# Kernel tuning notes

Hardware: AMD Instinct MI355X
Metric: run time of the kernel (lower is better)

The kernel has to match this reference:

```python
import jax, jax.numpy as jnp
import numpy as np

N_ENT = 100000
N_REL = 500
N_EDGES = 800000
IN_DIM = 128
OUT_DIM = 128


def setup_inputs() -> dict:
    key = jax.random.key(0)
    ks = jax.random.split(key, 7)
    heads = jax.random.randint(ks[0], (N_EDGES,), 0, N_ENT)
    tails = jax.random.randint(ks[1], (N_EDGES,), 0, N_ENT)
    rels = jax.random.randint(ks[2], (N_EDGES,), 0, N_REL)
    triplets = jnp.stack([heads, tails, rels], axis=1)  # [E, 3] (head, tail, rel)
    ent_embed = jax.random.normal(ks[3], (N_ENT, IN_DIM), dtype=jnp.float32)
    rel_embed = jax.random.normal(ks[4], (N_REL, IN_DIM), dtype=jnp.float32)
    # xavier_normal with gain=1.414 for both linear weights; zero biases (torch default bias init is uniform, but scale is tiny)
    Wa = jax.random.normal(ks[5], (OUT_DIM, 3 * IN_DIM), dtype=jnp.float32) * (1.414 * np.sqrt(2.0 / (3 * IN_DIM + OUT_DIM)))
    Wa2 = jax.random.normal(ks[6], (1, OUT_DIM), dtype=jnp.float32) * (1.414 * np.sqrt(2.0 / (OUT_DIM + 1)))
    ba = jnp.zeros((OUT_DIM,), dtype=jnp.float32)
    ba2 = jnp.zeros((1,), dtype=jnp.float32)
    return {"triplets": triplets, "ent_embed": ent_embed, "rel_embed": rel_embed,
            "Wa": Wa, "ba": ba, "Wa2": Wa2, "ba2": ba2}


def reference(triplets, ent_embed, rel_embed, Wa, ba, Wa2, ba2):
    heads = triplets[:, 0]
    tails = triplets[:, 1]
    rels = triplets[:, 2]
    # gather per-edge features: [E, 3*in_dim]
    h = jnp.concatenate([ent_embed[heads], rel_embed[rels], ent_embed[tails]], axis=1)
    c = h @ Wa.T + ba                      # [E, out_dim]
    b = jax.nn.leaky_relu(c @ Wa2.T + ba2)  # [E, 1], slope 0.01 (torch default)
    e_b = jnp.exp(b)                       # [E, 1]
    # torch builds sparse COO (head, rel) tensors, detaches, and sums over dim=1:
    # that is exactly a segment-sum over head node. detach -> stop_gradient.
    ebs = jax.ops.segment_sum(jax.lax.stop_gradient(e_b), heads, num_segments=N_ENT)       # [N, 1]
    hs = jax.ops.segment_sum(jax.lax.stop_gradient(e_b * c), heads, num_segments=N_ENT)    # [N, out_dim]
    ebs = jnp.where(ebs == 0.0, jnp.float32(1e-12), ebs)
    out = hs / ebs
    return jax.nn.elu(out)  # concat=True branch
```

## Files before the change

### kernel.cpp

```cpp
#include <hip/hip_runtime.h>

#define N_ENT   100000
#define N_REL   500
#define N_EDGES 800000
#define DIM     128
#define WA_LD   384

#define MT       256
#define ENT_BLKS ((N_ENT + MT - 1) / MT)
#define REL_BLKS 63
#define CAP      64

#define SCW 264

typedef __attribute__((ext_vector_type(8))) short  s8v;
typedef __attribute__((ext_vector_type(4))) float  f4v;

__device__ __forceinline__ unsigned short f2bf(float x) {
    unsigned u = __float_as_uint(x);
    return (unsigned short)((u + 0x7FFFu + ((u >> 16) & 1u)) >> 16);
}
__device__ __forceinline__ float bf2f(unsigned short h) {
    return __uint_as_float(((unsigned)h) << 16);
}

__global__ __launch_bounds__(256) void k_prep(const float* __restrict__ Wa,
                                              short* __restrict__ Bg) {
    int idx = blockIdx.x * 256 + threadIdx.x;
    int tt = idx >> 11;
    int g = idx & 2047;
    int j = g >> 4;
    int k8 = g & 15;
    const float* src = Wa + (size_t)j * WA_LD + tt * 256 + k8 * 8;
    float4 v0 = *(const float4*)src;
    float4 v1 = *(const float4*)(src + 4);
    float x[8] = {v0.x, v0.y, v0.z, v0.w, v1.x, v1.y, v1.z, v1.w};
    s8v hv;
#pragma unroll
    for (int e = 0; e < 8; ++e) hv[e] = (short)f2bf(x[e]);
    int col = tt * 128 + j;
    int kc = k8 >> 2;
    int lanep = (k8 & 3) * 16 + (col & 15);
    int nt = col >> 4;
    *(s8v*)&Bg[((size_t)((kc * 16 + nt) * 64 + lanep)) * 8] = hv;
}

__global__ __launch_bounds__(512) void k_fused(const float* __restrict__ ent,
                                               const short* __restrict__ Bg,
                                               const float* __restrict__ Wa2,
                                               unsigned short* __restrict__ PHb,
                                               unsigned short* __restrict__ PTb,
                                               float* __restrict__ qh,
                                               float* __restrict__ qt,
                                               const float* __restrict__ rel,
                                               const float* __restrict__ Wa,
                                               const float* __restrict__ ba,
                                               float* __restrict__ PR,
                                               float* __restrict__ qr) {
    __shared__ __align__(16) unsigned short SCR[8 * 16 * SCW];
    __shared__ float relLds[8][128];
    s8v* BsV = (s8v*)SCR;
    int t = threadIdx.x;
    int wv = t >> 6;
    int lane = t & 63;

    if (blockIdx.x >= ENT_BLKS) {
        int rb = blockIdx.x - ENT_BLKS;
        int r = rb * 8 + wv;
        if (r < N_REL) {
            relLds[wv][lane]      = rel[r * DIM + lane];
            relLds[wv][64 + lane] = rel[r * DIM + 64 + lane];
            int j0 = 2 * lane, j1 = j0 + 1;
            const float* w0 = Wa + (size_t)j0 * WA_LD + 128;
            const float* w1 = Wa + (size_t)j1 * WA_LD + 128;
            float a0 = ba[j0], a1 = ba[j1];
#pragma unroll 8
            for (int k4 = 0; k4 < 32; ++k4) {
                float4 rv = *(const float4*)&relLds[wv][4 * k4];
                float4 x0 = *(const float4*)&w0[4 * k4];
                float4 x1 = *(const float4*)&w1[4 * k4];
                a0 += rv.x * x0.x + rv.y * x0.y + rv.z * x0.z + rv.w * x0.w;
                a1 += rv.x * x1.x + rv.y * x1.y + rv.z * x1.z + rv.w * x1.w;
            }
            *(float2*)&PR[(size_t)r * DIM + j0] = make_float2(a0, a1);
            float p = a0 * Wa2[j0] + a1 * Wa2[j1];
#pragma unroll
            for (int m = 1; m <= 32; m <<= 1) p += __shfl_xor(p, m);
            if (lane == 0) qr[r] = p;
        }
        return;
    }

#pragma unroll
    for (int it = 0; it < 8; ++it) {
        int idx = t + 512 * it;
        BsV[idx] = *(const s8v*)&Bg[(size_t)idx * 8];
    }

    int l15 = lane & 15, lg = lane >> 4;
    int m0 = blockIdx.x * MT + wv * 32;

    f4v acc[2][16];
#pragma unroll
    for (int s = 0; s < 2; ++s)
#pragma unroll
        for (int nt = 0; nt < 16; ++nt)
            acc[s][nt] = (f4v){0.f, 0.f, 0.f, 0.f};

    __syncthreads();

#pragma unroll
    for (int kc = 0; kc < 4; ++kc) {
        s8v Ah[2];
#pragma unroll
        for (int s = 0; s < 2; ++s) {
            int row = m0 + s * 16 + l15;
            if (row < N_ENT) {
                const float* ap = ent + (size_t)row * DIM + kc * 32 + lg * 8;
                float4 v0 = *(const float4*)ap;
                float4 v1 = *(const float4*)(ap + 4);
                float x[8] = {v0.x, v0.y, v0.z, v0.w, v1.x, v1.y, v1.z, v1.w};
#pragma unroll
                for (int e = 0; e < 8; ++e) Ah[s][e] = (short)f2bf(x[e]);
            } else {
                Ah[s] = (s8v){0, 0, 0, 0, 0, 0, 0, 0};
            }
        }
#pragma unroll
        for (int nt = 0; nt < 16; ++nt) {
            s8v bg = BsV[(kc * 16 + nt) * 64 + lane];
            acc[0][nt] = __builtin_amdgcn_mfma_f32_16x16x32_bf16(Ah[0], bg, acc[0][nt], 0, 0, 0);
            acc[1][nt] = __builtin_amdgcn_mfma_f32_16x16x32_bf16(Ah[1], bg, acc[1][nt], 0, 0, 0);
        }
    }

    float wa2v[8];
#pragma unroll
    for (int c8 = 0; c8 < 8; ++c8) wa2v[c8] = Wa2[c8 * 16 + l15];

#pragma unroll
    for (int s = 0; s < 2; ++s) {
        int rowb = m0 + s * 16 + lg * 4;
        float qhp[4] = {0.f, 0.f, 0.f, 0.f};
        float qtp[4] = {0.f, 0.f, 0.f, 0.f};
#pragma unroll
        for (int nt = 0; nt < 16; ++nt) {
#pragma unroll
            for (int g = 0; g < 4; ++g) {
                float v = acc[s][nt][g];
                if (nt < 8) qhp[g] += v * wa2v[nt];
                else        qtp[g] += v * wa2v[nt & 7];
            }
        }
#pragma unroll
        for (int g = 0; g < 4; ++g) {
            float a = qhp[g], b = qtp[g];
#pragma unroll
            for (int m = 1; m <= 8; m <<= 1) {
                a += __shfl_xor(a, m);
                b += __shfl_xor(b, m);
            }
            int row = rowb + g;
            if (l15 == 0 && row < N_ENT) { qh[row] = a; qt[row] = b; }
        }
    }

    __syncthreads();

    unsigned short* scr = &SCR[wv * 16 * SCW];
#pragma unroll
    for (int s = 0; s < 2; ++s) {
#pragma unroll
        for (int nt = 0; nt < 16; ++nt)
#pragma unroll
            for (int g = 0; g < 4; ++g)
                scr[(lg * 4 + g) * SCW + nt * 16 + l15] = f2bf(acc[s][nt][g]);
#pragma unroll
        for (int p = 0; p < 8; ++p) {
            int row16 = p * 2 + (lane >> 5);
            int col8  = lane & 31;
            s8v val = *(s8v*)&scr[row16 * SCW + col8 * 8];
            int row = m0 + s * 16 + row16;
            if (row < N_ENT) {
                unsigned short* dst = (col8 < 16 ? PHb : PTb)
                                    + (size_t)row * DIM + (col8 & 15) * 8;
                *(s8v*)dst = val;
            }
        }
    }
}

__global__ __launch_bounds__(256) void k_scatter(const int* __restrict__ trip,
                                                 const float* __restrict__ qh,
                                                 const float* __restrict__ qt,
                                                 const float* __restrict__ qr,
                                                 const float* __restrict__ ba2,
                                                 int* __restrict__ cnt,
                                                 float2* __restrict__ pkw) {
    __shared__ int tl3[768];
    __shared__ float qrs[N_REL];
    int t = threadIdx.x;
    for (int i = t; i < N_REL; i += 256) qrs[i] = qr[i];
    int e0blk = blockIdx.x * 256;
    int base3 = e0blk * 3;
#pragma unroll
    for (int i = t; i < 768; i += 256)
        tl3[i] = (base3 + i < N_EDGES * 3) ? trip[base3 + i] : 0;
    __syncthreads();
    int e = e0blk + t;
    if (e >= N_EDGES) return;
    int h  = tl3[t * 3 + 0];
    int tt = tl3[t * 3 + 1];
    int r  = tl3[t * 3 + 2];
    float b = qh[h] + qt[tt] + qrs[r] + ba2[0];
    float lr = b > 0.f ? b : 0.01f * b;
    float w = expf(lr);
    int pos = atomicAdd(&cnt[h], 1);
    if (pos < CAP) {
        float2 v;
        v.x = __uint_as_float(((unsigned)r << 17) | (unsigned)tt);
        v.y = w;
        pkw[(size_t)h * CAP + pos] = v;
    }
}

__global__ __launch_bounds__(256) void k_gather(const int* __restrict__ cnt,
                                                const float2* __restrict__ pkw,
                                                const unsigned short* __restrict__ PHb,
                                                const float* __restrict__ PR,
                                                const unsigned short* __restrict__ PTb,
                                                float* __restrict__ out) {
    int idx = blockIdx.x * 256 + threadIdx.x;
    int i = idx >> 5, lane = idx & 31;
    if (i >= N_ENT) return;
    int lane4 = lane * 4;
    int e0 = i * CAP;
    int n = cnt[i]; if (n > CAP) n = CAP;
    int e1 = e0 + n;
    float4 acc = make_float4(0.f, 0.f, 0.f, 0.f);
    float sw = 0.f;
    int e = e0;
    for (; e + 3 < e1; e += 4) {
        float2 pw0 = pkw[e],     pw1 = pkw[e + 1];
        float2 pw2 = pkw[e + 2], pw3 = pkw[e + 3];
        unsigned p0 = __float_as_uint(pw0.x), p1 = __float_as_uint(pw1.x);
        unsigned p2 = __float_as_uint(pw2.x), p3 = __float_as_uint(pw3.x);
        ushort4 b0 = *(const ushort4*)&PTb[(size_t)(p0 & 0x1FFFFu) * DIM + lane4];
        ushort4 b1 = *(const ushort4*)&PTb[(size_t)(p1 & 0x1FFFFu) * DIM + lane4];
        ushort4 b2 = *(const ushort4*)&PTb[(size_t)(p2 & 0x1FFFFu) * DIM + lane4];
        ushort4 b3 = *(const ushort4*)&PTb[(size_t)(p3 & 0x1FFFFu) * DIM + lane4];
        float4 r0 = *(const float4*)&PR[(size_t)(p0 >> 17) * DIM + lane4];
        float4 r1 = *(const float4*)&PR[(size_t)(p1 >> 17) * DIM + lane4];
        float4 r2 = *(const float4*)&PR[(size_t)(p2 >> 17) * DIM + lane4];
        float4 r3 = *(const float4*)&PR[(size_t)(p3 >> 17) * DIM + lane4];
        float w0 = pw0.y, w1 = pw1.y, w2 = pw2.y, w3 = pw3.y;
        acc.x += w0 * (r0.x + bf2f(b0.x)) + w1 * (r1.x + bf2f(b1.x))
               + w2 * (r2.x + bf2f(b2.x)) + w3 * (r3.x + bf2f(b3.x));
        acc.y += w0 * (r0.y + bf2f(b0.y)) + w1 * (r1.y + bf2f(b1.y))
               + w2 * (r2.y + bf2f(b2.y)) + w3 * (r3.y + bf2f(b3.y));
        acc.z += w0 * (r0.z + bf2f(b0.z)) + w1 * (r1.z + bf2f(b1.z))
               + w2 * (r2.z + bf2f(b2.z)) + w3 * (r3.z + bf2f(b3.z));
        acc.w += w0 * (r0.w + bf2f(b0.w)) + w1 * (r1.w + bf2f(b1.w))
               + w2 * (r2.w + bf2f(b2.w)) + w3 * (r3.w + bf2f(b3.w));
        sw += (w0 + w1) + (w2 + w3);
    }
    for (; e < e1; ++e) {
        float2 pw = pkw[e];
        unsigned p = __float_as_uint(pw.x);
        float w = pw.y;
        ushort4 b = *(const ushort4*)&PTb[(size_t)(p & 0x1FFFFu) * DIM + lane4];
        float4 pr = *(const float4*)&PR[(size_t)(p >> 17) * DIM + lane4];
        acc.x += w * (pr.x + bf2f(b.x));
        acc.y += w * (pr.y + bf2f(b.y));
        acc.z += w * (pr.z + bf2f(b.z));
        acc.w += w * (pr.w + bf2f(b.w));
        sw += w;
    }
    ushort4 hb = *(const ushort4*)&PHb[(size_t)i * DIM + lane4];
    acc.x += sw * bf2f(hb.x);
    acc.y += sw * bf2f(hb.y);
    acc.z += sw * bf2f(hb.z);
    acc.w += sw * bf2f(hb.w);
    float den = (sw == 0.f) ? 1e-12f : sw;
    float inv = 1.f / den;
    float vx = acc.x * inv, vy = acc.y * inv, vz = acc.z * inv, vw = acc.w * inv;
    vx = vx > 0.f ? vx : expm1f(vx);
    vy = vy > 0.f ? vy : expm1f(vy);
    vz = vz > 0.f ? vz : expm1f(vz);
    vw = vw > 0.f ? vw : expm1f(vw);
    *(float4*)&out[(size_t)i * DIM + lane4] = make_float4(vx, vy, vz, vw);
}

extern "C" void kernel_launch(void* const* d_in, const int* in_sizes, int n_in,
                              void* d_out, int out_size, void* d_ws, size_t ws_size,
                              hipStream_t stream) {
    const int*   trip = (const int*)d_in[0];
    const float* ent  = (const float*)d_in[1];
    const float* rel  = (const float*)d_in[2];
    const float* Wa   = (const float*)d_in[3];
    const float* ba   = (const float*)d_in[4];
    const float* Wa2  = (const float*)d_in[5];
    const float* ba2  = (const float*)d_in[6];
    float* out = (float*)d_out;

    float* ws = (float*)d_ws;
    size_t o = 0;
    unsigned short* PHb = (unsigned short*)(ws + o); o += (size_t)N_ENT * DIM / 2;
    unsigned short* PTb = (unsigned short*)(ws + o); o += (size_t)N_ENT * DIM / 2;
    float* PR = ws + o;        o += (size_t)N_REL * DIM;
    float* qh = ws + o;        o += N_ENT;
    float* qt = ws + o;        o += N_ENT;
    float* qr = ws + o;        o += N_REL + 4;
    short* Bg = (short*)(ws + o);     o += 32768 / 2 + 8;
    int*   cnt = (int*)(ws + o);      o += N_ENT;
    float2* pkw = (float2*)(ws + o);  o += (size_t)N_ENT * CAP * 2;

    hipMemsetAsync(cnt, 0, (size_t)N_ENT * sizeof(int), stream);

    k_prep<<<16, 256, 0, stream>>>(Wa, Bg);
    k_fused<<<ENT_BLKS + REL_BLKS, 512, 0, stream>>>(ent, Bg, Wa2, PHb, PTb, qh, qt,
                                                     rel, Wa, ba, PR, qr);
    k_scatter<<<(N_EDGES + 255) / 256, 256, 0, stream>>>(trip, qh, qt, qr, ba2, cnt, pkw);
    k_gather<<<(N_ENT * 32) / 256, 256, 0, stream>>>(cnt, pkw, PHb, PR, PTb, out);
}
```

Measured before the change: 137.5 us.

## Split fused entity GEMM into two N-halves with smaller blocks

The entity projection kernel now uses 256-thread blocks covering 128 rows. It preloads all A fragments into registers, then runs two passes that each stage half of the bf16 weight tiles in LDS and compute 8 output tiles. This halves the live accumulator count and shrinks LDS per block, aiming for higher occupancy and more blocks in flight. The cost is extra barriers, reloading B per pass, and holding the whole A row in registers.

```diff
diff --git a/kernel.cpp b/kernel.cpp
--- a/kernel.cpp
+++ b/kernel.cpp
@@ -6,12 +6,12 @@
 #define DIM     128
 #define WA_LD   384
 
-#define MT       256
+#define MT       128
 #define ENT_BLKS ((N_ENT + MT - 1) / MT)
-#define REL_BLKS 63
+#define REL_BLKS 125
 #define CAP      64
 
-#define SCW 264
+#define SCW 144
 
 typedef __attribute__((ext_vector_type(8))) short  s8v;
 typedef __attribute__((ext_vector_type(4))) float  f4v;
@@ -45,7 +45,7 @@
     *(s8v*)&Bg[((size_t)((kc * 16 + nt) * 64 + lanep)) * 8] = hv;
 }
 
-__global__ __launch_bounds__(512) void k_fused(const float* __restrict__ ent,
+__global__ __launch_bounds__(256) void k_fused(const float* __restrict__ ent,
                                                const short* __restrict__ Bg,
                                                const float* __restrict__ Wa2,
                                                unsigned short* __restrict__ PHb,
@@ -57,16 +57,16 @@
                                                const float* __restrict__ ba,
                                                float* __restrict__ PR,
                                                float* __restrict__ qr) {
-    __shared__ __align__(16) unsigned short SCR[8 * 16 * SCW];
-    __shared__ float relLds[8][128];
-    s8v* BsV = (s8v*)SCR;
+    __shared__ __align__(16) s8v Bs[2048];
+    __shared__ __align__(16) unsigned short SCR[4 * 16 * SCW];
+    __shared__ float relLds[4][128];
     int t = threadIdx.x;
     int wv = t >> 6;
     int lane = t & 63;
 
     if (blockIdx.x >= ENT_BLKS) {
         int rb = blockIdx.x - ENT_BLKS;
-        int r = rb * 8 + wv;
+        int r = rb * 4 + wv;
         if (r < N_REL) {
             relLds[wv][lane]      = rel[r * DIM + lane];
             relLds[wv][64 + lane] = rel[r * DIM + 64 + lane];
@@ -91,100 +91,101 @@
         return;
     }
 
-#pragma unroll
-    for (int it = 0; it < 8; ++it) {
-        int idx = t + 512 * it;
-        BsV[idx] = *(const s8v*)&Bg[(size_t)idx * 8];
-    }
-
     int l15 = lane & 15, lg = lane >> 4;
     int m0 = blockIdx.x * MT + wv * 32;
 
-    f4v acc[2][16];
-#pragma unroll
-    for (int s = 0; s < 2; ++s)
-#pragma unroll
-        for (int nt = 0; nt < 16; ++nt)
-            acc[s][nt] = (f4v){0.f, 0.f, 0.f, 0.f};
-
-    __syncthreads();
-
-#pragma unroll
-    for (int kc = 0; kc < 4; ++kc) {
-        s8v Ah[2];
+    s8v Af[2][4];
+#pragma unroll
+    for (int s = 0; s < 2; ++s) {
+        int row = m0 + s * 16 + l15;
+        if (row < N_ENT) {
+            const float* ap = ent + (size_t)row * DIM + lg * 8;
+#pragma unroll
+            for (int kc = 0; kc < 4; ++kc) {
+                float4 v0 = *(const float4*)(ap + kc * 32);
+                float4 v1 = *(const float4*)(ap + kc * 32 + 4);
+                float x[8] = {v0.x, v0.y, v0.z, v0.w, v1.x, v1.y, v1.z, v1.w};
+#pragma unroll
+                for (int e = 0; e < 8; ++e) Af[s][kc][e] = (short)f2bf(x[e]);
+            }
+        } else {
+#pragma unroll
+            for (int kc = 0; kc < 4; ++kc)
+                Af[s][kc] = (s8v){0, 0, 0, 0, 0, 0, 0, 0};
+        }
+    }
+
+    float wa2v[8];
+#pragma unroll
+    for (int c8 = 0; c8 < 8; ++c8) wa2v[c8] = Wa2[c8 * 16 + l15];
+
+    const s8v* Bg8 = (const s8v*)Bg;
+    unsigned short* scr = &SCR[wv * 16 * SCW];
+
+#pragma unroll
+    for (int pass = 0; pass < 2; ++pass) {
+#pragma unroll
+        for (int it = 0; it < 8; ++it) {
+            int g = t + 256 * it;
+            int tile = g >> 6, l = g & 63;
+            int kc = tile >> 3, ntl = tile & 7;
+            Bs[g] = Bg8[(kc * 16 + pass * 8 + ntl) * 64 + l];
+        }
+        __syncthreads();
+
+        f4v acc[2][8];
+#pragma unroll
+        for (int s = 0; s < 2; ++s)
+#pragma unroll
+            for (int nt = 0; nt < 8; ++nt)
+                acc[s][nt] = (f4v){0.f, 0.f, 0.f, 0.f};
+
+#pragma unroll
+        for (int kc = 0; kc < 4; ++kc)
+#pragma unroll
+            for (int nt = 0; nt < 8; ++nt) {
+                s8v bg = Bs[(kc * 8 + nt) * 64 + lane];
+                acc[0][nt] = __builtin_amdgcn_mfma_f32_16x16x32_bf16(Af[0][kc], bg, acc[0][nt], 0, 0, 0);
+                acc[1][nt] = __builtin_amdgcn_mfma_f32_16x16x32_bf16(Af[1][kc], bg, acc[1][nt], 0, 0, 0);
+            }
+        __syncthreads();
+
+        float* qd = pass ? qt : qh;
+        unsigned short* Pb = pass ? PTb : PHb;
 #pragma unroll
         for (int s = 0; s < 2; ++s) {
-            int row = m0 + s * 16 + l15;
-            if (row < N_ENT) {
-                const float* ap = ent + (size_t)row * DIM + kc * 32 + lg * 8;
-                float4 v0 = *(const float4*)ap;
-                float4 v1 = *(const float4*)(ap + 4);
-                float x[8] = {v0.x, v0.y, v0.z, v0.w, v1.x, v1.y, v1.z, v1.w};
-#pragma unroll
-                for (int e = 0; e < 8; ++e) Ah[s][e] = (short)f2bf(x[e]);
-            } else {
-                Ah[s] = (s8v){0, 0, 0, 0, 0, 0, 0, 0};
-            }
-        }
-#pragma unroll
-        for (int nt = 0; nt < 16; ++nt) {
-            s8v bg = BsV[(kc * 16 + nt) * 64 + lane];
-            acc[0][nt] = __builtin_amdgcn_mfma_f32_16x16x32_bf16(Ah[0], bg, acc[0][nt], 0, 0, 0);
-            acc[1][nt] = __builtin_amdgcn_mfma_f32_16x16x32_bf16(Ah[1], bg, acc[1][nt], 0, 0, 0);
-        }
-    }
-
-    float wa2v[8];
-#pragma unroll
-    for (int c8 = 0; c8 < 8; ++c8) wa2v[c8] = Wa2[c8 * 16 + l15];
-
-#pragma unroll
-    for (int s = 0; s < 2; ++s) {
-        int rowb = m0 + s * 16 + lg * 4;
-        float qhp[4] = {0.f, 0.f, 0.f, 0.f};
-        float qtp[4] = {0.f, 0.f, 0.f, 0.f};
-#pragma unroll
-        for (int nt = 0; nt < 16; ++nt) {
+            int rowb = m0 + s * 16 + lg * 4;
+            float qp[4] = {0.f, 0.f, 0.f, 0.f};
+#pragma unroll
+            for (int nt = 0; nt < 8; ++nt)
+#pragma unroll
+                for (int g = 0; g < 4; ++g)
+                    qp[g] += acc[s][nt][g] * wa2v[nt];
 #pragma unroll
             for (int g = 0; g < 4; ++g) {
-                float v = acc[s][nt][g];
-                if (nt < 8) qhp[g] += v * wa2v[nt];
-                else        qtp[g] += v * wa2v[nt & 7];
-            }
-        }
-#pragma unroll
-        for (int g = 0; g < 4; ++g) {
-            float a = qhp[g], b = qtp[g];
-#pragma unroll
-            for (int m = 1; m <= 8; m <<= 1) {
-                a += __shfl_xor(a, m);
-                b += __shfl_xor(b, m);
-            }
-            int row = rowb + g;
-            if (l15 == 0 && row < N_ENT) { qh[row] = a; qt[row] = b; }
-        }
-    }
-
-    __syncthreads();
-
-    unsigned short* scr = &SCR[wv * 16 * SCW];
-#pragma unroll
-    for (int s = 0; s < 2; ++s) {
-#pragma unroll
-        for (int nt = 0; nt < 16; ++nt)
-#pragma unroll
-            for (int g = 0; g < 4; ++g)
-                scr[(lg * 4 + g) * SCW + nt * 16 + l15] = f2bf(acc[s][nt][g]);
-#pragma unroll
-        for (int p = 0; p < 8; ++p) {
-            int row16 = p * 2 + (lane >> 5);
-            int col8  = lane & 31;
-            s8v val = *(s8v*)&scr[row16 * SCW + col8 * 8];
-            int row = m0 + s * 16 + row16;
-            if (row < N_ENT) {
-                unsigned short* dst = (col8 < 16 ? PHb : PTb)
-                                    + (size_t)row * DIM + (col8 & 15) * 8;
-                *(s8v*)dst = val;
+                float a = qp[g];
+#pragma unroll
+                for (int m = 1; m <= 8; m <<= 1) a += __shfl_xor(a, m);
+                int row = rowb + g;
+                if (l15 == 0 && row < N_ENT) qd[row] = a;
+            }
+        }
+
+#pragma unroll
+        for (int s = 0; s < 2; ++s) {
+#pragma unroll
+            for (int nt = 0; nt < 8; ++nt)
+#pragma unroll
+                for (int g = 0; g < 4; ++g)
+                    scr[(lg * 4 + g) * SCW + nt * 16 + l15] = f2bf(acc[s][nt][g]);
+#pragma unroll
+            for (int p = 0; p < 4; ++p) {
+                int c = p * 64 + lane;
+                int row16 = c >> 4, col8 = c & 15;
+                s8v val = *(s8v*)&scr[row16 * SCW + col8 * 8];
+                int row = m0 + s * 16 + row16;
+                if (row < N_ENT)
+                    *(s8v*)&Pb[(size_t)row * DIM + col8 * 8] = val;
             }
         }
     }
@@ -318,7 +319,7 @@
     hipMemsetAsync(cnt, 0, (size_t)N_ENT * sizeof(int), stream);
 
     k_prep<<<16, 256, 0, stream>>>(Wa, Bg);
-    k_fused<<<ENT_BLKS + REL_BLKS, 512, 0, stream>>>(ent, Bg, Wa2, PHb, PTb, qh, qt,
+    k_fused<<<ENT_BLKS + REL_BLKS, 256, 0, stream>>>(ent, Bg, Wa2, PHb, PTb, qh, qt,
                                                      rel, Wa, ba, PR, qr);
     k_scatter<<<(N_EDGES + 255) / 256, 256, 0, stream>>>(trip, qh, qt, qr, ba2, cnt, pkw);
     k_gather<<<(N_ENT * 32) / 256, 256, 0, stream>>>(cnt, pkw, PHb, PR, PTb, out);
```

After: 144.2 us. 1.05x slower.
